# Optimization experiments

Measured on AMD Instinct MI355X. Metric: run time of the kernel, lower is better.

The kernel has to match this reference:

```python
import jax, jax.numpy as jnp
import numpy as np


def setup_inputs() -> dict:
    key = jax.random.key(0)
    k1, k2 = jax.random.split(key)
    B, C, H, W = 32, 8, 256, 256
    inp = jax.random.normal(k1, (B, C, H, W), dtype=jnp.float32)
    tgt = jax.random.uniform(k2, (B, C, H, W), dtype=jnp.float32)
    return {"input": inp, "target": tgt}


def reference(input, target):
    B, C, H, W = input.shape
    # normalized coordinate grids: (index+1)/size, as in the original loops
    x_grid = (jnp.arange(W, dtype=input.dtype) + 1.0) / W          # [W]
    y_grid = (jnp.arange(H, dtype=input.dtype) + 1.0) / H          # [H]

    # per-(b,c) softmax over the flattened heatmap (DSNT)
    p = jax.nn.softmax(input.reshape(B, C, H * W), axis=-1).reshape(B, C, H, W)
    pred_x = jnp.einsum('bchw,w->bc', p, x_grid)                   # [B, C]
    pred_y = jnp.einsum('bchw,h->bc', p, y_grid)                   # [B, C]

    # ground-truth coords from argmax of target heatmap
    idx = jnp.argmax(target.reshape(B, C, H * W), axis=-1)         # [B, C] int
    true_x = ((idx % W) + 1).astype(input.dtype) / W
    true_y = ((idx // W) + 1).astype(input.dtype) / H

    ed = jnp.sqrt((true_x - pred_x) ** 2 + (true_y - pred_y) ** 2)  # [B, C]
    # original sums over all (batch, channel) pairs, divides by batch size only
    return jnp.sum(ed) / B
```

## Files before the change

kernel.cpp:

```cpp
#include <hip/hip_runtime.h>
#include <math.h>


constexpr int HW    = 256 * 256;
constexpr int BLOCK = 256;
constexpr int SPLIT = 16;
constexpr int CHUNK4 = (HW / 4) / SPLIT;
constexpr int ITERS  = CHUNK4 / BLOCK;

__global__ __launch_bounds__(BLOCK, 8) void dsnt_partial_kernel(
        const float* __restrict__ input,
        const float* __restrict__ target,
        unsigned long long* __restrict__ ws_pk,
        float* __restrict__ ws_s,
        float* __restrict__ ws_sx,
        float* __restrict__ ws_sy)
{
    const int bc    = blockIdx.x >> 4;
    const int chunk = blockIdx.x & (SPLIT - 1);
    const int tid   = threadIdx.x;

    const float4* __restrict__ in4 =
        reinterpret_cast<const float4*>(input) + (size_t)bc * (HW / 4) + chunk * CHUNK4;
    const float4* __restrict__ tg4 =
        reinterpret_cast<const float4*>(target) + (size_t)bc * (HW / 4) + chunk * CHUNK4;

    const float4 v0 = in4[tid];              const float4 t0 = tg4[tid];
    const float4 v1 = in4[tid + BLOCK];      const float4 t1 = tg4[tid + BLOCK];
    const float4 v2 = in4[tid + 2 * BLOCK];  const float4 t2 = tg4[tid + 2 * BLOCK];
    const float4 v3 = in4[tid + 3 * BLOCK];  const float4 t3 = tg4[tid + 3 * BLOCK];
    __builtin_amdgcn_sched_barrier(0);

    float s = 0.f, sx = 0.f, sy = 0.f;
    float bv = -INFINITY;
    int   bi = 0x7FFFFFFF;

    const int fbase = 4 * chunk * CHUNK4;

#define DSNT_STEP(V, T, OFF)                                              \
    {                                                                     \
        const int f = fbase + 4 * (tid + (OFF));                          \
        const float y  = (float)((f >> 8) + 1) * (1.0f / 256.0f);         \
        const float x0 = (float)((f & 255) + 1) * (1.0f / 256.0f);        \
        const float e0 = __expf(V.x);                                     \
        const float e1 = __expf(V.y);                                     \
        const float e2 = __expf(V.z);                                     \
        const float e3 = __expf(V.w);                                     \
        const float es = (e0 + e1) + (e2 + e3);                           \
        s  += es;                                                         \
        sy += es * y;                                                     \
        sx += e0 * x0                                                     \
            + e1 * (x0 + 1.0f / 256.0f)                                   \
            + e2 * (x0 + 2.0f / 256.0f)                                   \
            + e3 * (x0 + 3.0f / 256.0f);                                  \
        if (T.x > bv) { bv = T.x; bi = f; }                               \
        if (T.y > bv) { bv = T.y; bi = f + 1; }                           \
        if (T.z > bv) { bv = T.z; bi = f + 2; }                           \
        if (T.w > bv) { bv = T.w; bi = f + 3; }                           \
    }

    DSNT_STEP(v0, t0, 0 * BLOCK)
    DSNT_STEP(v1, t1, 1 * BLOCK)
    DSNT_STEP(v2, t2, 2 * BLOCK)
    DSNT_STEP(v3, t3, 3 * BLOCK)
#undef DSNT_STEP

    unsigned long long pk =
        ((unsigned long long)__float_as_uint(bv) << 32) |
        (unsigned long long)(0xFFFFFFFFu - (unsigned)bi);

    #pragma unroll
    for (int off = 32; off > 0; off >>= 1) {
        s  += __shfl_down(s, off);
        sx += __shfl_down(sx, off);
        sy += __shfl_down(sy, off);
        const unsigned long long opk = __shfl_down(pk, off);
        pk = (opk > pk) ? opk : pk;
    }

    __shared__ float ls[4], lsx[4], lsy[4];
    __shared__ unsigned long long lpk[4];
    const int wave = tid >> 6;
    const int lane = tid & 63;
    if (lane == 0) {
        ls[wave]  = s;
        lsx[wave] = sx;
        lsy[wave] = sy;
        lpk[wave] = pk;
    }
    __syncthreads();

    if (tid == 0) {
        #pragma unroll
        for (int wv = 1; wv < 4; ++wv) {
            s  += ls[wv];
            sx += lsx[wv];
            sy += lsy[wv];
            pk = (lpk[wv] > pk) ? lpk[wv] : pk;
        }
        const int slot = blockIdx.x;
        ws_s[slot]  = s;
        ws_sx[slot] = sx;
        ws_sy[slot] = sy;
        ws_pk[slot] = pk;
    }
}

__global__ __launch_bounds__(256) void dsnt_final_kernel(
        const unsigned long long* __restrict__ ws_pk,
        const float* __restrict__ ws_s,
        const float* __restrict__ ws_sx,
        const float* __restrict__ ws_sy,
        float* __restrict__ out,
        int nmap)
{
    const int bc = threadIdx.x;
    float ed = 0.f;
    if (bc < nmap) {
        float s = 0.f, sx = 0.f, sy = 0.f;
        unsigned long long pk = 0ull;
        #pragma unroll
        for (int c = 0; c < SPLIT; ++c) {
            const int slot = bc * SPLIT + c;
            s  += ws_s[slot];
            sx += ws_sx[slot];
            sy += ws_sy[slot];
            const unsigned long long p = ws_pk[slot];
            pk = (p > pk) ? p : pk;
        }
        const unsigned bi = 0xFFFFFFFFu - (unsigned)(pk & 0xFFFFFFFFull);
        const float px = sx / s;
        const float py = sy / s;
        const float tx = (float)((bi & 255) + 1) * (1.0f / 256.0f);
        const float ty = (float)((bi >> 8) + 1) * (1.0f / 256.0f);
        const float dx = tx - px;
        const float dy = ty - py;
        ed = sqrtf(dx * dx + dy * dy);
    }

    #pragma unroll
    for (int off = 32; off > 0; off >>= 1)
        ed += __shfl_down(ed, off);

    __shared__ float led[4];
    const int wave = threadIdx.x >> 6;
    const int lane = threadIdx.x & 63;
    if (lane == 0) led[wave] = ed;
    __syncthreads();

    if (threadIdx.x == 0) {
        const float total = (led[0] + led[1]) + (led[2] + led[3]);
        out[0] = total * (1.0f / 32.0f);
    }
}

extern "C" void kernel_launch(void* const* d_in, const int* in_sizes, int n_in,
                              void* d_out, int out_size, void* d_ws, size_t ws_size,
                              hipStream_t stream) {
    const float* input  = (const float*)d_in[0];
    const float* target = (const float*)d_in[1];
    float* out = (float*)d_out;

    const int n_maps = in_sizes[0] / HW;
    const int nslot  = n_maps * SPLIT;

    unsigned long long* ws_pk = (unsigned long long*)d_ws;
    float* ws_s  = (float*)((char*)d_ws + (size_t)8  * nslot);
    float* ws_sx = (float*)((char*)d_ws + (size_t)12 * nslot);
    float* ws_sy = (float*)((char*)d_ws + (size_t)16 * nslot);

    dsnt_partial_kernel<<<nslot, BLOCK, 0, stream>>>(input, target,
                                                     ws_pk, ws_s, ws_sx, ws_sy);
    dsnt_final_kernel<<<1, 256, 0, stream>>>(ws_pk, ws_s, ws_sx, ws_sy,
                                             out, n_maps);
}
```

Baseline: 144.8 us.

## Stream target via global_load_lds and overlap softmax with staged waits

The target tiles are now loaded directly into LDS with global_load_lds, and the input loads are issued through inline asm with immediate offsets. Partial vmcnt waits let the exp/sum work on each input vector start as soon as that vector arrives. The argmax scan then runs over the LDS copy of the target. This is meant to free VGPRs and overlap compute with outstanding memory traffic, at the cost of 16KB of LDS per block, a lower occupancy hint, and fragile hand-counted vmcnt values.

```diff
diff --git a/kernel.cpp b/kernel.cpp
--- a/kernel.cpp
+++ b/kernel.cpp
@@ -8,7 +8,7 @@
 constexpr int CHUNK4 = (HW / 4) / SPLIT;
 constexpr int ITERS  = CHUNK4 / BLOCK;
 
-__global__ __launch_bounds__(BLOCK, 8) void dsnt_partial_kernel(
+__global__ __launch_bounds__(BLOCK, 6) void dsnt_partial_kernel(
         const float* __restrict__ input,
         const float* __restrict__ target,
         unsigned long long* __restrict__ ws_pk,
@@ -19,17 +19,38 @@
     const int bc    = blockIdx.x >> 4;
     const int chunk = blockIdx.x & (SPLIT - 1);
     const int tid   = threadIdx.x;
+    const int wave  = tid >> 6;
+    const int lane  = tid & 63;
 
     const float4* __restrict__ in4 =
         reinterpret_cast<const float4*>(input) + (size_t)bc * (HW / 4) + chunk * CHUNK4;
     const float4* __restrict__ tg4 =
         reinterpret_cast<const float4*>(target) + (size_t)bc * (HW / 4) + chunk * CHUNK4;
 
-    const float4 v0 = in4[tid];              const float4 t0 = tg4[tid];
-    const float4 v1 = in4[tid + BLOCK];      const float4 t1 = tg4[tid + BLOCK];
-    const float4 v2 = in4[tid + 2 * BLOCK];  const float4 t2 = tg4[tid + 2 * BLOCK];
-    const float4 v3 = in4[tid + 3 * BLOCK];  const float4 t3 = tg4[tid + 3 * BLOCK];
-    __builtin_amdgcn_sched_barrier(0);
+    __shared__ float4 lt[CHUNK4];
+
+    const char* in_lo = (const char*)(in4 + tid) + 2048;
+    const char* in_hi = (const char*)(in4 + tid) + 10240;
+
+    float4 v0, v1, v2, v3;
+    asm volatile(
+        "global_load_dwordx4 %0, %4, off offset:-2048\n\t"
+        "global_load_dwordx4 %1, %4, off offset:2048\n\t"
+        "global_load_dwordx4 %2, %5, off offset:-2048\n\t"
+        "global_load_dwordx4 %3, %5, off offset:2048"
+        : "=&v"(v0), "=&v"(v1), "=&v"(v2), "=&v"(v3)
+        : "v"(in_lo), "v"(in_hi)
+        : "memory");
+
+    #pragma unroll
+    for (int c = 0; c < ITERS; ++c) {
+        const float4* gsrc = tg4 + c * BLOCK + tid;
+        float4* ldst = &lt[c * BLOCK + (wave << 6)];
+        __builtin_amdgcn_global_load_lds(
+            (const __attribute__((address_space(1))) void*)gsrc,
+            (__attribute__((address_space(3))) void*)ldst,
+            16, 0, 0);
+    }
 
     float s = 0.f, sx = 0.f, sy = 0.f;
     float bv = -INFINITY;
@@ -37,7 +58,11 @@
 
     const int fbase = 4 * chunk * CHUNK4;
 
-#define DSNT_STEP(V, T, OFF)                                              \
+#define DSNT_WAIT(N)                                                      \
+    asm volatile("s_waitcnt vmcnt(" #N ")" ::: "memory");                 \
+    __builtin_amdgcn_sched_barrier(0);
+
+#define DSNT_SM_STEP(V, OFF)                                              \
     {                                                                     \
         const int f = fbase + 4 * (tid + (OFF));                          \
         const float y  = (float)((f >> 8) + 1) * (1.0f / 256.0f);         \
@@ -53,17 +78,26 @@
             + e1 * (x0 + 1.0f / 256.0f)                                   \
             + e2 * (x0 + 2.0f / 256.0f)                                   \
             + e3 * (x0 + 3.0f / 256.0f);                                  \
-        if (T.x > bv) { bv = T.x; bi = f; }                               \
-        if (T.y > bv) { bv = T.y; bi = f + 1; }                           \
-        if (T.z > bv) { bv = T.z; bi = f + 2; }                           \
-        if (T.w > bv) { bv = T.w; bi = f + 3; }                           \
-    }
-
-    DSNT_STEP(v0, t0, 0 * BLOCK)
-    DSNT_STEP(v1, t1, 1 * BLOCK)
-    DSNT_STEP(v2, t2, 2 * BLOCK)
-    DSNT_STEP(v3, t3, 3 * BLOCK)
-#undef DSNT_STEP
+    }
+
+    DSNT_WAIT(7) DSNT_SM_STEP(v0, 0 * BLOCK)
+    DSNT_WAIT(6) DSNT_SM_STEP(v1, 1 * BLOCK)
+    DSNT_WAIT(5) DSNT_SM_STEP(v2, 2 * BLOCK)
+    DSNT_WAIT(4) DSNT_SM_STEP(v3, 3 * BLOCK)
+
+    DSNT_WAIT(0)
+#undef DSNT_SM_STEP
+#undef DSNT_WAIT
+
+    #pragma unroll
+    for (int c = 0; c < ITERS; ++c) {
+        const float4 t = lt[c * BLOCK + tid];
+        const int f = fbase + 4 * (tid + c * BLOCK);
+        if (t.x > bv) { bv = t.x; bi = f; }
+        if (t.y > bv) { bv = t.y; bi = f + 1; }
+        if (t.z > bv) { bv = t.z; bi = f + 2; }
+        if (t.w > bv) { bv = t.w; bi = f + 3; }
+    }
 
     unsigned long long pk =
         ((unsigned long long)__float_as_uint(bv) << 32) |
@@ -80,8 +114,6 @@
 
     __shared__ float ls[4], lsx[4], lsy[4];
     __shared__ unsigned long long lpk[4];
-    const int wave = tid >> 6;
-    const int lane = tid & 63;
     if (lane == 0) {
         ls[wave]  = s;
         lsx[wave] = sx;
```

Result: no change. 145.2 us (+0.3%).
